# Kernel tuning notes

Hardware: AMD Instinct MI355X
Metric: run time of the kernel (lower is better)

The kernel has to match this reference:

```python
import jax, jax.numpy as jnp
import numpy as np

N = 20000          # total nodes across batched graphs
E_REL = 60000      # edges per relation type (3 relation types)
N_CLASSES = 32
NUM_GRAPHS = 64
HEADS = 8
OUT_CH = 48
FUSED = 384        # 3 * 128 fused node feature dim
EPS = 1e-5         # PyG LayerNorm eps
NEG_SLOPE = 0.2    # RGATConv leaky_relu slope
NUM_ITERS = 2


def setup_inputs() -> dict:
    key = jax.random.key(0)
    ks = iter(jax.random.split(key, 48))

    def nrm(shape, scale=0.05):
        return jax.random.normal(next(ks), shape, jnp.float32) * scale

    inp = {}
    inp["x_visual"] = jax.random.normal(next(ks), (N, 1024), jnp.float32)
    inp["x_geom"] = jax.random.normal(next(ks), (N, 6), jnp.float32)
    inp["x_prior"] = jax.random.uniform(next(ks), (N, N_CLASSES + 1), jnp.float32)
    inp["edge_index_overlap"] = jax.random.randint(next(ks), (2, E_REL), 0, N)
    inp["edge_index_arch"] = jax.random.randint(next(ks), (2, E_REL), 0, N)
    inp["edge_index_spatial"] = jax.random.randint(next(ks), (2, E_REL), 0, N)
    inp["batch"] = jnp.sort(jax.random.randint(next(ks), (N,), 0, NUM_GRAPHS))
    # encoders: Linear -> ReLU -> PyG LayerNorm(graph mode, batch=None)
    inp["vis_W"] = nrm((1024, 128)); inp["vis_b"] = jnp.zeros((128,), jnp.float32)
    inp["vis_lnw"] = jnp.ones((128,), jnp.float32); inp["vis_lnb"] = jnp.zeros((128,), jnp.float32)
    inp["geo_W"] = nrm((6, 128)); inp["geo_b"] = jnp.zeros((128,), jnp.float32)
    inp["geo_lnw"] = jnp.ones((128,), jnp.float32); inp["geo_lnb"] = jnp.zeros((128,), jnp.float32)
    inp["pri_W"] = nrm((N_CLASSES + 1, 128)); inp["pri_b"] = jnp.zeros((128,), jnp.float32)
    inp["pri_lnw"] = jnp.ones((128,), jnp.float32); inp["pri_lnb"] = jnp.zeros((128,), jnp.float32)
    # RGATConv params: weight (R, in, H*O), q/k (H*O, H*dim) with dim=1, bias (H*O)
    for i in (1, 2):
        inp[f"rgat{i}_W"] = nrm((3, FUSED, HEADS * OUT_CH))
        inp[f"rgat{i}_q"] = nrm((HEADS * OUT_CH, HEADS))
        inp[f"rgat{i}_k"] = nrm((HEADS * OUT_CH, HEADS))
        inp[f"rgat{i}_bias"] = jnp.zeros((HEADS * OUT_CH,), jnp.float32)
        inp[f"n{i}_w"] = jnp.ones((FUSED,), jnp.float32)
        inp[f"n{i}_b"] = jnp.zeros((FUSED,), jnp.float32)
    inp["cls_W1"] = nrm((FUSED, 128)); inp["cls_b1"] = jnp.zeros((128,), jnp.float32)
    inp["cls_W2"] = nrm((128, N_CLASSES)); inp["cls_b2"] = jnp.zeros((N_CLASSES,), jnp.float32)
    return inp


def _encoder(x, W, b, lnw, lnb):
    # Linear -> ReLU -> PyG LayerNorm(mode='graph', batch=None): scalar mean/std
    h = jax.nn.relu(x @ W + b)
    h = h - h.mean()
    h = h / (h.std() + EPS)
    return h * lnw + lnb


def _graph_layernorm(x, batch, w, b):
    # PyG LayerNorm(mode='graph') with batch vector: normalize per graph over nodes*channels
    cnt = jax.ops.segment_sum(jnp.ones((x.shape[0],), x.dtype), batch, NUM_GRAPHS)
    norm = jnp.clip(cnt, 1.0, None) * x.shape[-1]
    mean = jax.ops.segment_sum(x, batch, NUM_GRAPHS).sum(-1) / norm
    xc = x - mean[batch][:, None]
    var = jax.ops.segment_sum(xc * xc, batch, NUM_GRAPHS).sum(-1) / norm
    out = xc / jnp.sqrt(var + EPS)[batch][:, None]
    return out * w + b


def _rgat(x, src, dst, etype, W, q, k, bias):
    # RGATConv: additive self-attention, across-relation softmax, concat heads, sum aggr
    n = x.shape[0]
    xr = jnp.einsum('nf,rfo->rno', x, W)          # per-relation node transform (R,N,H*O)
    outi = xr[etype, dst]                          # (E, H*O) transformed dst features
    outj = xr[etype, src]                          # (E, H*O) transformed src features
    alpha = jax.nn.leaky_relu(outi @ q + outj @ k, NEG_SLOPE)  # (E, H)
    amax = jax.ops.segment_max(alpha, dst, n)
    amax = jnp.where(jnp.isfinite(amax), amax, 0.0)
    ex = jnp.exp(alpha - amax[dst])
    den = jax.ops.segment_sum(ex, dst, n)
    a = ex / (den[dst] + 1e-16)                    # per-dst-node softmax over all relations
    msg = (a[:, :, None] * outj.reshape(-1, HEADS, OUT_CH)).reshape(-1, HEADS * OUT_CH)
    return jax.ops.segment_sum(msg, dst, n) + bias


def reference(x_visual, x_geom, x_prior, edge_index_overlap, edge_index_arch,
              edge_index_spatial, batch, vis_W, vis_b, vis_lnw, vis_lnb,
              geo_W, geo_b, geo_lnw, geo_lnb, pri_W, pri_b, pri_lnw, pri_lnb,
              rgat1_W, rgat1_q, rgat1_k, rgat1_bias, n1_w, n1_b,
              rgat2_W, rgat2_q, rgat2_k, rgat2_bias, n2_w, n2_b,
              cls_W1, cls_b1, cls_W2, cls_b2):
    ei = jnp.concatenate([edge_index_overlap, edge_index_arch, edge_index_spatial], axis=1)
    src, dst = ei[0], ei[1]
    etype = jnp.concatenate([jnp.full((E_REL,), r, jnp.int32) for r in range(3)])

    h_vis = _encoder(x_visual, vis_W, vis_b, vis_lnw, vis_lnb)
    h_geo = _encoder(x_geom, geo_W, geo_b, geo_lnw, geo_lnb)

    cur_prior = x_prior
    logits = None
    for t in range(NUM_ITERS):
        h_pri = _encoder(cur_prior, pri_W, pri_b, pri_lnw, pri_lnb)
        h0 = jnp.concatenate([h_vis, h_geo, h_pri], axis=-1)  # (N, 384)
        h1 = jax.nn.elu(_rgat(h0, src, dst, etype, rgat1_W, rgat1_q, rgat1_k, rgat1_bias)) + h0
        h1 = _graph_layernorm(h1, batch, n1_w, n1_b)
        h2 = jax.nn.elu(_rgat(h1, src, dst, etype, rgat2_W, rgat2_q, rgat2_k, rgat2_bias)) + h1
        h2 = _graph_layernorm(h2, batch, n2_w, n2_b)
        logits = jax.nn.relu(h2 @ cls_W1 + cls_b1) @ cls_W2 + cls_b2  # dropout off (eval)
        if t < NUM_ITERS - 1:
            probs = jax.nn.softmax(logits, axis=-1)
            cur_prior = jnp.concatenate([probs, probs.max(-1, keepdims=True)], axis=-1)
    return logits
```

## Files before the change

### kernel.cpp

```cpp
#include <hip/hip_runtime.h>
#include <hip/hip_bf16.h>

#define Nn 20000
#define EREL 60000
#define ETOT 180000
#define NG 64
#define FD 384
#define EPS 1e-5f

typedef unsigned short u16;
typedef unsigned int u32;
typedef __attribute__((ext_vector_type(8))) short s8v;
typedef __attribute__((ext_vector_type(4))) float f4v;

static inline int cdiv(int a, int b) { return (a + b - 1) / b; }

__device__ inline u16 f2b(float f) {
    __hip_bfloat16 h = __float2bfloat16(f);
    union { __hip_bfloat16 b; u16 u; } c; c.b = h; return c.u;
}
__device__ inline float b2f(u16 u) {
    union { __hip_bfloat16 b; u16 u; } c; c.u = u; return __bfloat162float(c.b);
}

__global__ __launch_bounds__(256) void split_k(const float* __restrict__ x,
    u16* __restrict__ hi, u16* __restrict__ lo, int n4)
{
    int i = blockIdx.x * 256 + threadIdx.x;
    if (i >= n4) return;
    float4 v = ((const float4*)x)[i];
    ushort4 h, l;
    h.x = f2b(v.x); l.x = f2b(v.x - b2f(h.x));
    h.y = f2b(v.y); l.y = f2b(v.y - b2f(h.y));
    h.z = f2b(v.z); l.z = f2b(v.z - b2f(h.z));
    h.w = f2b(v.w); l.w = f2b(v.w - b2f(h.w));
    ((ushort4*)hi)[i] = h;
    ((ushort4*)lo)[i] = l;
}

__global__ void tsplit_k(const float* __restrict__ W, u16* __restrict__ hi,
                         u16* __restrict__ lo, int K, int N, int total)
{
    int idx = blockIdx.x * 256 + threadIdx.x;
    if (idx >= total) return;
    int kn = K * N;
    int b = idx / kn, rem = idx - b * kn;
    int k = rem / N, n = rem - k * N;
    float v = W[idx];
    u16 h = f2b(v), l = f2b(v - b2f(h));
    int o = b * kn + n * K + k;
    hi[o] = h; lo[o] = l;
}

__global__ void prep_qkw_k(const float* __restrict__ q, const float* __restrict__ kk,
                           u16* __restrict__ hi, u16* __restrict__ lo)
{
    int idx = blockIdx.x * 256 + threadIdx.x;
    if (idx >= 16 * 384) return;
    int col = idx / 384, k = idx - col * 384;
    float v = (col < 8) ? q[k * 8 + col] : kk[k * 8 + col - 8];
    u16 h = f2b(v), l = f2b(v - b2f(h));
    hi[idx] = h; lo[idx] = l;
}

#define USEI(i) ((i) < 2 || ((i) >= 4 && (i) < 6) || (TERMS >= 2 && ((i) == 2 || (i) == 3)) || (TERMS >= 3 && (i) >= 6))
template<bool BIAS, bool RELU, bool STATS, bool OB16, int TERMS, bool SWZ>
__global__ __launch_bounds__(256) void mgemm_k(
    const u16* __restrict__ Ahi, const u16* __restrict__ Alo,
    const u16* __restrict__ Bhi, const u16* __restrict__ Blo,
    const float* __restrict__ bias, void* __restrict__ Cv,
    int M, int K, int ldc, int bstride, float* __restrict__ stats)
{
    __shared__ u16 lds[4 * 128 * 32];
    __shared__ float red[256];
    const int t = threadIdx.x;
    int brow, bcol, z;
    if (SWZ) {
        int d = blockIdx.x;
        int xcd = d & 7, s = d >> 3;
        int row = xcd + 8 * (s / 9);
        int c = s % 9;
        brow = row * 128;
        if (brow >= M) return;
        bcol = (c % 3) * 128;
        z = c / 3;
    } else {
        brow = blockIdx.x * 128; bcol = blockIdx.y * 128; z = blockIdx.z;
    }
    Bhi += (size_t)z * bstride;
    Blo += (size_t)z * bstride;
    float* Cf = OB16 ? nullptr : (float*)Cv + (size_t)z * M * ldc;
    u16*   Ch = OB16 ? (u16*)Cv + (size_t)z * M * ldc : nullptr;

    const int r0 = t >> 2, sl = t & 3;
    const int rA0 = min(brow + r0, M - 1);
// ... 65 lines not shown
    float s1 = 0.f, s2 = 0.f;
    #pragma unroll
    for (int tm = 0; tm < 4; tm++) {
        #pragma unroll
        for (int rg = 0; rg < 4; rg++) {
            int row = brow + wr + tm * 16 + kq * 4 + rg;
            if (row < M) {
                #pragma unroll
                for (int tn = 0; tn < 4; tn++) {
                    int col = bcol + wc + tn * 16 + lr;
                    float v = acc[tm][tn][rg];
                    if (BIAS) v += bias[col];
                    if (RELU) v = fmaxf(v, 0.f);
                    if (OB16) Ch[(size_t)row * ldc + col] = f2b(v);
                    else      Cf[(size_t)row * ldc + col] = v;
                    if (STATS) { s1 += v; s2 += v * v; }
                }
            }
        }
    }
    if (STATS) {
        __syncthreads();
        red[t] = s1; __syncthreads();
        for (int o = 128; o; o >>= 1) { if (t < o) red[t] += red[t + o]; __syncthreads(); }
        if (t == 0) atomicAdd(&stats[0], red[0]);
        __syncthreads();
        red[t] = s2; __syncthreads();
        for (int o = 128; o; o >>= 1) { if (t < o) red[t] += red[t + o]; __syncthreads(); }
        if (t == 0) atomicAdd(&stats[1], red[0]);
    }
}
#undef USEI

__global__ __launch_bounds__(256) void proj_k(const u16* __restrict__ xr,
    const u16* __restrict__ qkw_hi, const u16* __restrict__ qkw_lo,
    float* __restrict__ qik)
{
    const int M3 = 3 * Nn;
    __shared__ u16 a_lds[128 * 32];
    __shared__ u16 b_lds[2][16 * 392];
    int t = threadIdx.x;
    int brow = blockIdx.x * 128;

    for (int i = t; i < 768; i += 256) {
        int col = i / 48, c8 = (i - col * 48) * 8;
        *(s8v*)&b_lds[0][col * 392 + c8] = *(const s8v*)(qkw_hi + col * 384 + c8);
        *(s8v*)&b_lds[1][col * 392 + c8] = *(const s8v*)(qkw_lo + col * 384 + c8);
    }

    int ar = t >> 1;
    int sl0 = (t & 1) * 2;
    int grow = min(brow + ar, M3 - 1);
    const u16* asrc = xr + (size_t)grow * 384;
    int adst0 = ar * 32 + ((sl0 ^ (ar & 3)) << 3);
    int adst1 = ar * 32 + (((sl0 + 1) ^ (ar & 3)) << 3);

    int l = t & 63, w = t >> 6;
    int lr = l & 15, kq = l >> 4;
    f4v acc0 = {}, acc1 = {};

    s8v stg0 = *(const s8v*)(asrc + sl0 * 8);
    s8v stg1 = *(const s8v*)(asrc + sl0 * 8 + 8);
    for (int kc = 0; kc < 12; kc++) {
        if (kc) __syncthreads();
        *(s8v*)&a_lds[adst0] = stg0;
        *(s8v*)&a_lds[adst1] = stg1;
        __syncthreads();
        if (kc + 1 < 12) {
            int ko = (kc + 1) * 32 + sl0 * 8;
            stg0 = *(const s8v*)(asrc + ko);
            stg1 = *(const s8v*)(asrc + ko + 8);
        }
        s8v bh = *(const s8v*)&b_lds[0][lr * 392 + kc * 32 + kq * 8];
        s8v bl = *(const s8v*)&b_lds[1][lr * 392 + kc * 32 + kq * 8];
        int r0 = w * 32 + lr;
        s8v a0 = *(const s8v*)&a_lds[r0 * 32 + ((kq ^ (r0 & 3)) << 3)];
        int r1 = r0 + 16;
        s8v a1 = *(const s8v*)&a_lds[r1 * 32 + ((kq ^ (r1 & 3)) << 3)];
        acc0 = __builtin_amdgcn_mfma_f32_16x16x32_bf16(a0, bh, acc0, 0, 0, 0);
        acc0 = __builtin_amdgcn_mfma_f32_16x16x32_bf16(a0, bl, acc0, 0, 0, 0);
        acc1 = __builtin_amdgcn_mfma_f32_16x16x32_bf16(a1, bh, acc1, 0, 0, 0);
        acc1 = __builtin_amdgcn_mfma_f32_16x16x32_bf16(a1, bl, acc1, 0, 0, 0);
    }
    #pragma unroll
    for (int rg = 0; rg < 4; rg++) {
        int row0 = brow + w * 32 + kq * 4 + rg;
        if (row0 < M3) qik[(size_t)row0 * 16 + lr] = acc0[rg];
        int row1 = row0 + 16;
        if (row1 < M3) qik[(size_t)row1 * 16 + lr] = acc1[rg];
    }
}

template<bool BIAS, bool RELU, bool STATS>
__global__ __launch_bounds__(256) void sgemm_k(
    const float* __restrict__ A, const float* __restrict__ B,
    const float* __restrict__ bias, float* __restrict__ C,
    int M, int K, int N, int ldc, float* __restrict__ stats)
{
    const int BK = 16;
    const int r = blockIdx.z;
    B += (size_t)r * K * N;
    C += (size_t)r * M * ldc;
    __shared__ float As[16][65];
    __shared__ float Bs[16][64];
    int tid = threadIdx.x;
    int tx = tid & 15, ty = tid >> 4;
    int brow = blockIdx.x * 64, bcol = blockIdx.y * 64;
    float acc[4][4] = {};
    for (int k0 = 0; k0 < K; k0 += BK) {
        #pragma unroll
        for (int i = 0; i < 4; i++) {
            int e = tid + 256 * i;
            int ar = e >> 4, ak = e & 15;
            int gr = brow + ar, gk = k0 + ak;
            As[ak][ar] = (gr < M && gk < K) ? A[(size_t)gr * K + gk] : 0.f;
            int bk = e >> 6, bn = e & 63;
            int gbk = k0 + bk, gbn = bcol + bn;
            Bs[bk][bn] = (gbk < K && gbn < N) ? B[(size_t)gbk * N + gbn] : 0.f;
        }
        __syncthreads();
        #pragma unroll
        for (int k = 0; k < BK; k++) {
            float ra[4], rb[4];
// ... 29 lines not shown
        __shared__ float red[256];
        __syncthreads();
        red[tid] = s1; __syncthreads();
        for (int o = 128; o; o >>= 1) { if (tid < o) red[tid] += red[tid + o]; __syncthreads(); }
        if (tid == 0) atomicAdd(&stats[0], red[0]);
        __syncthreads();
        red[tid] = s2; __syncthreads();
        for (int o = 128; o; o >>= 1) { if (tid < o) red[tid] += red[tid + o]; __syncthreads(); }
        if (tid == 0) atomicAdd(&stats[1], red[0]);
    }
}

__global__ __launch_bounds__(256) void enc_norm_k(const float* __restrict__ H,
                           const float* __restrict__ w, const float* __restrict__ b,
                           const float* __restrict__ stats, float cntinv, u16* __restrict__ hi)
{
    int i = blockIdx.x * 256 + threadIdx.x;
    if (i >= Nn * 32) return;
    int n = i >> 5, c4 = i & 31;
    float m = stats[0] * cntinv;
    float var = stats[1] * cntinv - m * m;
    float s = 1.f / (sqrtf(fmaxf(var, 0.f)) + EPS);
    float4 wv = ((const float4*)w)[c4];
    float4 bv = ((const float4*)b)[c4];
    float4 v = ((const float4*)(H + (size_t)n * FD))[c4];
    ushort4 hh;
    hh.x = f2b((v.x - m) * s * wv.x + bv.x);
    hh.y = f2b((v.y - m) * s * wv.y + bv.y);
    hh.z = f2b((v.z - m) * s * wv.z + bv.z);
    hh.w = f2b((v.w - m) * s * wv.w + bv.w);
    ((ushort4*)(hi + (size_t)n * FD))[c4] = hh;
}

__global__ __launch_bounds__(256) void ew_k(const float* __restrict__ qik,
    const int* __restrict__ eidx, const int* __restrict__ dste, float* __restrict__ ew)
{
    int e = blockIdx.x * 256 + threadIdx.x;
    if (e >= ETOT) return;
    int p = eidx[e];
    int src = p & 0xFFFFFF, et = p >> 24;
    int dst = dste[e];
    const float4* q4 = (const float4*)(qik + ((size_t)et * Nn + dst) * 16);
    const float4* k4 = (const float4*)(qik + ((size_t)et * Nn + src) * 16 + 8);
    float4 out[2];
    #pragma unroll
    for (int half = 0; half < 2; half++) {
        float4 qv = q4[half], kv = k4[half];
        float a0 = qv.x + kv.x, a1 = qv.y + kv.y, a2 = qv.z + kv.z, a3 = qv.w + kv.w;
        a0 = (a0 > 0.f) ? a0 : 0.2f * a0;
        a1 = (a1 > 0.f) ? a1 : 0.2f * a1;
        a2 = (a2 > 0.f) ? a2 : 0.2f * a2;
        a3 = (a3 > 0.f) ? a3 : 0.2f * a3;
        out[half] = make_float4(__expf(a0), __expf(a1), __expf(a2), __expf(a3));
    }
    float4* ew4 = (float4*)(ew + (size_t)e * 8);
    ew4[0] = out[0];
    ew4[1] = out[1];
}

__global__ void edge_count_k(const int* __restrict__ e0, const int* __restrict__ e1,
                             const int* __restrict__ e2, int* __restrict__ cnt)
{
    int e = blockIdx.x * 256 + threadIdx.x;
    if (e >= ETOT) return;
    int r = e / EREL, i = e - r * EREL;
    const int* ei = (r == 0) ? e0 : (r == 1) ? e1 : e2;
    atomicAdd(&cnt[ei[EREL + i]], 1);
}

__global__ void edge_fill_k(const int* __restrict__ e0, const int* __restrict__ e1,
                            const int* __restrict__ e2, int* __restrict__ cursor,
                            int* __restrict__ eidx, int* __restrict__ dste)
{
    int e = blockIdx.x * 256 + threadIdx.x;
    if (e >= ETOT) return;
    int r = e / EREL, i = e - r * EREL;
    const int* ei = (r == 0) ? e0 : (r == 1) ? e1 : e2;
    int src = ei[i], dst = ei[EREL + i];
    int pos = atomicAdd(&cursor[dst], 1);
    eidx[pos] = src | (r << 24);
    dste[pos] = dst;
}

__global__ __launch_bounds__(1024) void scan_k(const int* __restrict__ cnt,
                                               int* __restrict__ rowptr, int* __restrict__ cursor)
{
    __shared__ int wsum[16], wpre[16];
    __shared__ int carry, tot;
    int t = threadIdx.x, lane = t & 63, wid = t >> 6;
    if (t == 0) carry = 0;
    __syncthreads();
    for (int base = 0; base < Nn; base += 1024) {
        int i = base + t;
        int v = (i < Nn) ? cnt[i] : 0;
        int s = v;
        #pragma unroll
        for (int o = 1; o < 64; o <<= 1) {
            int x = __shfl_up(s, o);
            if (lane >= o) s += x;
        }
        if (lane == 63) wsum[wid] = s;
        __syncthreads();
        if (t < 16) {
            int wv = wsum[t];
            int ws = wv;
            #pragma unroll
            for (int o = 1; o < 16; o <<= 1) {
                int x = __shfl_up(ws, o);
                if (t >= o) ws += x;
            }
            wpre[t] = ws - wv;
            if (t == 15) tot = ws;
        }
        __syncthreads();
        if (i < Nn) {
            int ex = carry + wpre[wid] + s - v;
            rowptr[i] = ex; cursor[i] = ex;
        }
        __syncthreads();
        if (t == 0) carry += tot;
    }
    __syncthreads();
    if (t == 0) rowptr[Nn] = carry;
}

__global__ __launch_bounds__(256) void gcount_k(const int* __restrict__ batch, int* __restrict__ gcnt)
{
    __shared__ int bins[NG];
    int t = threadIdx.x;
    if (t < NG) bins[t] = 0;
    __syncthreads();
    int n = blockIdx.x * 256 + t;
    if (n < Nn) atomicAdd(&bins[batch[n]], 1);
    __syncthreads();
    if (t < NG && bins[t]) atomicAdd(&gcnt[t], bins[t]);
}

__global__ __launch_bounds__(256) void aggr_k(const u16* __restrict__ xr,
    const float* __restrict__ ew, const int* __restrict__ rowptr, const int* __restrict__ eidx,
    const float* __restrict__ bias, const u16* __restrict__ hinb,
    const int* __restrict__ batch, u16* __restrict__ outb,
    float* __restrict__ gsum, float* __restrict__ gsq)
{
    __shared__ float ls[NG], lq[NG];
    int t = threadIdx.x;
    if (t < NG) { ls[t] = 0.f; lq[t] = 0.f; }
    __syncthreads();
    int node = blockIdx.x * 4 + (t >> 6);
    int lane = t & 63;
    int e0 = rowptr[node], e1 = rowptr[node + 1];
    int hd[3];
    #pragma unroll
    for (int j = 0; j < 3; j++) hd[j] = (lane * 2 + 128 * j) / 48;
    float den = 0.f;
    float accx[3] = {}, accy[3] = {};

    int e = e0;
    while (e + 4 <= e1) {
        int p0 = eidx[e], p1 = eidx[e + 1], p2 = eidx[e + 2], p3 = eidx[e + 3];
        const u32* r0 = (const u32*)(xr + ((size_t)(p0 >> 24) * Nn + (p0 & 0xFFFFFF)) * FD);
        const u32* r1 = (const u32*)(xr + ((size_t)(p1 >> 24) * Nn + (p1 & 0xFFFFFF)) * FD);
        const u32* r2 = (const u32*)(xr + ((size_t)(p2 >> 24) * Nn + (p2 & 0xFFFFFF)) * FD);
        const u32* r3 = (const u32*)(xr + ((size_t)(p3 >> 24) * Nn + (p3 & 0xFFFFFF)) * FD);
        float ev0 = (lane < 8) ? ew[(size_t)e * 8 + lane] : 0.f;
        float ev1 = (lane < 8) ? ew[(size_t)(e + 1) * 8 + lane] : 0.f;
        float ev2 = (lane < 8) ? ew[(size_t)(e + 2) * 8 + lane] : 0.f;
        float ev3 = (lane < 8) ? ew[(size_t)(e + 3) * 8 + lane] : 0.f;
        u32 u0[3], u1[3], u2[3], u3[3];
        #pragma unroll
        for (int j = 0; j < 3; j++) u0[j] = r0[lane + 64 * j];
        #pragma unroll
        for (int j = 0; j < 3; j++) u1[j] = r1[lane + 64 * j];
        #pragma unroll
        for (int j = 0; j < 3; j++) u2[j] = r2[lane + 64 * j];
        #pragma unroll
        for (int j = 0; j < 3; j++) u3[j] = r3[lane + 64 * j];
        den += ev0 + ev1 + ev2 + ev3;
        #pragma unroll
        for (int j = 0; j < 3; j++) {
            float a0 = __shfl(ev0, hd[j]), a1 = __shfl(ev1, hd[j]);
            float a2 = __shfl(ev2, hd[j]), a3 = __shfl(ev3, hd[j]);
            accx[j] = fmaf(a0, __uint_as_float(u0[j] << 16), accx[j]);
            accy[j] = fmaf(a0, __uint_as_float(u0[j] & 0xffff0000u), accy[j]);
            accx[j] = fmaf(a1, __uint_as_float(u1[j] << 16), accx[j]);
            accy[j] = fmaf(a1, __uint_as_float(u1[j] & 0xffff0000u), accy[j]);
            accx[j] = fmaf(a2, __uint_as_float(u2[j] << 16), accx[j]);
            accy[j] = fmaf(a2, __uint_as_float(u2[j] & 0xffff0000u), accy[j]);
            accx[j] = fmaf(a3, __uint_as_float(u3[j] << 16), accx[j]);
            accy[j] = fmaf(a3, __uint_as_float(u3[j] & 0xffff0000u), accy[j]);
        }
        e += 4;
    }
    for (; e < e1; e++) {
        int p = eidx[e];
        int srcn = p & 0xFFFFFF, et = p >> 24;
        float ev = (lane < 8) ? ew[(size_t)e * 8 + lane] : 0.f;
        den += ev;
        const u32* row = (const u32*)(xr + ((size_t)et * Nn + srcn) * FD);
        #pragma unroll
        for (int j = 0; j < 3; j++) {
            float a = __shfl(ev, hd[j]);
            u32 u = row[lane + 64 * j];
            accx[j] = fmaf(a, __uint_as_float(u << 16), accx[j]);
            accy[j] = fmaf(a, __uint_as_float(u & 0xffff0000u), accy[j]);
        }
    }

    float s1 = 0.f, s2 = 0.f;
    #pragma unroll
    for (int j = 0; j < 3; j++) {
        float dh = __shfl(den, hd[j]);
        float rcp = 1.f / (dh + 1e-16f);
        int c = lane * 2 + 128 * j;
        float2 bv = *(const float2*)(bias + c);
        u32 hb = ((const u32*)(hinb + (size_t)node * FD))[lane + 64 * j];
        float vx = accx[j] * rcp + bv.x;
        float vy = accy[j] * rcp + bv.y;
        vx = (vx > 0.f) ? vx : expm1f(vx);
        vy = (vy > 0.f) ? vy : expm1f(vy);
        vx += b2f((u16)(hb & 0xffffu));
        vy += b2f((u16)(hb >> 16));
        u32 pb = (u32)f2b(vx) | ((u32)f2b(vy) << 16);
        ((u32*)(outb + (size_t)node * FD))[lane + 64 * j] = pb;
        s1 += vx + vy; s2 += vx * vx + vy * vy;
    }
    #pragma unroll
    for (int o = 32; o; o >>= 1) { s1 += __shfl_down(s1, o); s2 += __shfl_down(s2, o); }
    int g = batch[node];
    if (lane == 0) { atomicAdd(&ls[g], s1); atomicAdd(&lq[g], s2); }
    __syncthreads();
    if (t < NG && (ls[t] != 0.f || lq[t] != 0.f)) {
        atomicAdd(&gsum[t], ls[t]);
        atomicAdd(&gsq[t], lq[t]);
    }
}

template<bool WLO>
__global__ __launch_bounds__(256) void gnorm_split_k(const u16* __restrict__ yb,
    const int* __restrict__ batch, const float* __restrict__ gsum, const float* __restrict__ gsq,
    const int* __restrict__ gcnt, const float* __restrict__ w, const float* __restrict__ b,
    u16* __restrict__ hi, u16* __restrict__ lo)
{
    int i = blockIdx.x * 256 + threadIdx.x;
    if (i >= Nn * (FD / 4)) return;
    int n = i / 96;
    int c4 = i - n * 96;
    int g = batch[n];
    float norm = fmaxf((float)gcnt[g], 1.f) * (float)FD;
    float m = gsum[g] / norm;
    float var = gsq[g] / norm - m * m;
    float rstd = rsqrtf(var + EPS);
    float4 wv = ((const float4*)w)[c4];
    float4 bv = ((const float4*)b)[c4];
    uint2 yv = ((const uint2*)yb)[i];
    float v0 = (b2f((u16)(yv.x & 0xffffu)) - m) * rstd * wv.x + bv.x;
    float v1 = (b2f((u16)(yv.x >> 16))     - m) * rstd * wv.y + bv.y;
// ... 34 lines not shown
                              hipStream_t stream)
{
    const float* x_visual = (const float*)d_in[0];
    const float* x_geom   = (const float*)d_in[1];
    const float* x_prior  = (const float*)d_in[2];
    const int* ei0   = (const int*)d_in[3];
    const int* ei1   = (const int*)d_in[4];
    const int* ei2   = (const int*)d_in[5];
    const int* batch = (const int*)d_in[6];
    const float* vis_W = (const float*)d_in[7];  const float* vis_b = (const float*)d_in[8];
    const float* vis_lnw = (const float*)d_in[9]; const float* vis_lnb = (const float*)d_in[10];
    const float* geo_W = (const float*)d_in[11]; const float* geo_b = (const float*)d_in[12];
    const float* geo_lnw = (const float*)d_in[13]; const float* geo_lnb = (const float*)d_in[14];
    const float* pri_W = (const float*)d_in[15]; const float* pri_b = (const float*)d_in[16];
    const float* pri_lnw = (const float*)d_in[17]; const float* pri_lnb = (const float*)d_in[18];
    const float* rgat_W[2]    = { (const float*)d_in[19], (const float*)d_in[25] };
    const float* rgat_q[2]    = { (const float*)d_in[20], (const float*)d_in[26] };
    const float* rgat_kk[2]   = { (const float*)d_in[21], (const float*)d_in[27] };
    const float* rgat_bias[2] = { (const float*)d_in[22], (const float*)d_in[28] };
    const float* ln_w[2]      = { (const float*)d_in[23], (const float*)d_in[29] };
    const float* ln_b[2]      = { (const float*)d_in[24], (const float*)d_in[30] };
    const float* cls_W1 = (const float*)d_in[31]; const float* cls_b1 = (const float*)d_in[32];
    const float* cls_W2 = (const float*)d_in[33]; const float* cls_b2 = (const float*)d_in[34];
    float* OUT = (float*)d_out;

    float* ws = (float*)d_ws;
    float* XRreg = ws;
    u16*   XR16  = (u16*)XRreg;
    float* HCAT  = XRreg + (size_t)3 * Nn * FD;
    float* HA    = HCAT + (size_t)Nn * FD;
    float* HB    = HA + (size_t)Nn * FD;
    float* PRIOR = HB + (size_t)Nn * FD;
    float* QIK   = PRIOR + (size_t)Nn * 33;
    u16* HS0_HI  = (u16*)(QIK + (size_t)3 * Nn * 16);
    u16* HS0_LO  = HS0_HI + (size_t)Nn * FD;
    u16* HS1_HI  = HS0_LO + (size_t)Nn * FD;
    u16* HS1_LO  = HS1_HI + (size_t)Nn * FD;
    u16* RW_HI   = HS1_LO + (size_t)Nn * FD;
    u16* RW_LO   = RW_HI + (size_t)2 * 3 * 384 * 384;
    u16* VW_HI   = RW_LO + (size_t)2 * 3 * 384 * 384;
    u16* VW_LO   = VW_HI + (size_t)128 * 1024;
    u16* CW_HI   = VW_LO + (size_t)128 * 1024;
    u16* CW_LO   = CW_HI + (size_t)128 * 384;
    u16* QKW_HI  = CW_LO + (size_t)128 * 384;
    u16* QKW_LO  = QKW_HI + (size_t)2 * 16 * 384;
    float* STATS = (float*)(QKW_LO + (size_t)2 * 16 * 384);
    float* GSUM  = STATS + 2;
    float* GSQ   = GSUM + 64;
    int* CNT    = (int*)(GSQ + 64);
    int* ROWPTR = CNT + Nn;
    int* CURSOR = ROWPTR + Nn + 1;
    int* EIDX   = CURSOR + Nn;
    int* GCNT   = EIDX + ETOT;
    int* DSTE   = GCNT + 64;
    float* EW   = (float*)(DSTE + ETOT);
    u16* VA_HI = (u16*)XRreg;
    u16* VA_LO = VA_HI + (size_t)Nn * 1024;
    float* CLSH = XRreg;
    u16* HS2_HI = (u16*)(XRreg + (size_t)12 * 1000 * 1000);
    u16* HS2_LO = HS2_HI + (size_t)Nn * FD;
    u16* YB0 = (u16*)HA;
    u16* YB1 = (u16*)HB;

    hipMemsetAsync(CNT, 0, Nn * sizeof(int), stream);
    edge_count_k<<<cdiv(ETOT, 256), 256, 0, stream>>>(ei0, ei1, ei2, CNT);
    scan_k<<<1, 1024, 0, stream>>>(CNT, ROWPTR, CURSOR);
    edge_fill_k<<<cdiv(ETOT, 256), 256, 0, stream>>>(ei0, ei1, ei2, CURSOR, EIDX, DSTE);
    hipMemsetAsync(GCNT, 0, 64 * sizeof(int), stream);
    gcount_k<<<cdiv(Nn, 256), 256, 0, stream>>>(batch, GCNT);

    tsplit_k<<<cdiv(3 * 384 * 384, 256), 256, 0, stream>>>(rgat_W[0], RW_HI, RW_LO, 384, 384, 3 * 384 * 384);
    tsplit_k<<<cdiv(3 * 384 * 384, 256), 256, 0, stream>>>(rgat_W[1], RW_HI + 3 * 384 * 384, RW_LO + 3 * 384 * 384, 384, 384, 3 * 384 * 384);
    tsplit_k<<<cdiv(1024 * 128, 256), 256, 0, stream>>>(vis_W, VW_HI, VW_LO, 1024, 128, 1024 * 128);
    tsplit_k<<<cdiv(384 * 128, 256), 256, 0, stream>>>(cls_W1, CW_HI, CW_LO, 384, 128, 384 * 128);
    prep_qkw_k<<<cdiv(16 * 384, 256), 256, 0, stream>>>(rgat_q[0], rgat_kk[0], QKW_HI, QKW_LO);
    prep_qkw_k<<<cdiv(16 * 384, 256), 256, 0, stream>>>(rgat_q[1], rgat_kk[1], QKW_HI + 16 * 384, QKW_LO + 16 * 384);
    split_k<<<cdiv(Nn * 1024 / 4, 256), 256, 0, stream>>>(x_visual, VA_HI, VA_LO, Nn * 1024 / 4);

    const int MB = cdiv(Nn, 128);
    const int XRBLK = 160 * 9;

    hipMemsetAsync(STATS, 0, 2 * sizeof(float), stream);
    mgemm_k<true, true, true, false, 2, false><<<dim3(MB, 1, 1), 256, 0, stream>>>(
        VA_HI, VA_LO, VW_HI, VW_LO, vis_b, HCAT, Nn, 1024, FD, 0, STATS);
    enc_norm_k<<<cdiv(Nn * 32, 256), 256, 0, stream>>>(HCAT, vis_lnw, vis_lnb, STATS, 1.f / ((float)Nn * 128.f), HS0_HI);

    dim3 genc(cdiv(Nn, 64), 2, 1);
    hipMemsetAsync(STATS, 0, 2 * sizeof(float), stream);
    sgemm_k<true, true, true><<<genc, 256, 0, stream>>>(x_geom, geo_W, geo_b, HCAT + 128, Nn, 6, 128, FD, STATS);
    enc_norm_k<<<cdiv(Nn * 32, 256), 256, 0, stream>>>(HCAT + 128, geo_lnw, geo_lnb, STATS, 1.f / ((float)Nn * 128.f), HS0_HI + 128);

    for (int t = 0; t < 2; t++) {
        const float* pin = t ? PRIOR : x_prior;
        hipMemsetAsync(STATS, 0, 2 * sizeof(float), stream);
        sgemm_k<true, true, true><<<genc, 256, 0, stream>>>(pin, pri_W, pri_b, HCAT + 256, Nn, 33, 128, FD, STATS);
        enc_norm_k<<<cdiv(Nn * 32, 256), 256, 0, stream>>>(HCAT + 256, pri_lnw, pri_lnb, STATS, 1.f / ((float)Nn * 128.f), HS0_HI + 256);

        for (int L = 0; L < 2; L++) {
            const u16* ahi = L ? HS1_HI : HS0_HI;
            const u16* alo = L ? HS1_LO : HS0_LO;
            u16* yout = L ? YB1 : YB0;
            mgemm_k<false, false, false, true, 1, true><<<dim3(XRBLK, 1, 1), 256, 0, stream>>>(
                ahi, alo, RW_HI + (size_t)L * 3 * 384 * 384, RW_LO + (size_t)L * 3 * 384 * 384,
                nullptr, XR16, Nn, 384, FD, 384 * 384, nullptr);
            proj_k<<<cdiv(3 * Nn, 128), 256, 0, stream>>>(XR16,
                QKW_HI + (size_t)L * 16 * 384, QKW_LO + (size_t)L * 16 * 384, QIK);
            ew_k<<<cdiv(ETOT, 256), 256, 0, stream>>>(QIK, EIDX, DSTE, EW);
            hipMemsetAsync(GSUM, 0, 128 * sizeof(float), stream);
            aggr_k<<<cdiv(Nn, 4), 256, 0, stream>>>(XR16, EW, ROWPTR, EIDX, rgat_bias[L],
                                                    ahi, batch, yout, GSUM, GSQ);
            if (L == 0)
                gnorm_split_k<false><<<cdiv(Nn * 96, 256), 256, 0, stream>>>(
                    YB0, batch, GSUM, GSQ, GCNT, ln_w[0], ln_b[0], HS1_HI, HS1_LO);
            else
                gnorm_split_k<true><<<cdiv(Nn * 96, 256), 256, 0, stream>>>(
                    YB1, batch, GSUM, GSQ, GCNT, ln_w[1], ln_b[1], HS2_HI, HS2_LO);
        }

        mgemm_k<true, true, false, false, 3, false><<<dim3(MB, 1, 1), 256, 0, stream>>>(
            HS2_HI, HS2_LO, CW_HI, CW_LO, cls_b1, CLSH, Nn, 384, 128, 0, nullptr);
        sgemm_k<true, false, false><<<dim3(cdiv(Nn, 64), 1, 1), 256, 0, stream>>>(
            CLSH, cls_W2, cls_b2, OUT, Nn, 128, 32, 32, nullptr);

        if (t == 0)
            softmax_prior_k<<<cdiv(Nn, 8), 256, 0, stream>>>(OUT, PRIOR);
    }
}
```

Before: 803.8 us.

## Fold q/k into RGAT weights, fuse edge scores into aggregation, drop lo-splits

Precomputes W·q and W·k per relation so the attention projections come straight from the input features (projh_k) rather than from the transformed features. The separate per-edge weight kernel and its dst array are removed, and attention logits and exponentials are now computed inside the aggregation kernel. The aggregation also switches to a contiguous lane*3 feature layout. Low bf16 residual splits are dropped for the visual input and RGAT weights, and the visual GEMM goes from two terms to one, which cuts preprocessing and GEMM work at some cost in precision.

```diff
diff --git a/kernel.cpp b/kernel.cpp
--- a/kernel.cpp
+++ b/kernel.cpp
@@ -23,21 +23,27 @@
     union { __hip_bfloat16 b; u16 u; } c; c.u = u; return __bfloat162float(c.b);
 }
 
+template<bool WLO>
 __global__ __launch_bounds__(256) void split_k(const float* __restrict__ x,
     u16* __restrict__ hi, u16* __restrict__ lo, int n4)
 {
     int i = blockIdx.x * 256 + threadIdx.x;
     if (i >= n4) return;
     float4 v = ((const float4*)x)[i];
-    ushort4 h, l;
-    h.x = f2b(v.x); l.x = f2b(v.x - b2f(h.x));
-    h.y = f2b(v.y); l.y = f2b(v.y - b2f(h.y));
-    h.z = f2b(v.z); l.z = f2b(v.z - b2f(h.z));
-    h.w = f2b(v.w); l.w = f2b(v.w - b2f(h.w));
+    ushort4 h;
+    h.x = f2b(v.x); h.y = f2b(v.y); h.z = f2b(v.z); h.w = f2b(v.w);
     ((ushort4*)hi)[i] = h;
-    ((ushort4*)lo)[i] = l;
-}
-
+    if (WLO) {
+        ushort4 l;
+        l.x = f2b(v.x - b2f(h.x));
+        l.y = f2b(v.y - b2f(h.y));
+        l.z = f2b(v.z - b2f(h.z));
+        l.w = f2b(v.w - b2f(h.w));
+        ((ushort4*)lo)[i] = l;
+    }
+}
+
+template<bool WLO>
 __global__ void tsplit_k(const float* __restrict__ W, u16* __restrict__ hi,
                          u16* __restrict__ lo, int K, int N, int total)
 {
@@ -47,20 +53,33 @@
     int b = idx / kn, rem = idx - b * kn;
     int k = rem / N, n = rem - k * N;
     float v = W[idx];
-    u16 h = f2b(v), l = f2b(v - b2f(h));
+    u16 h = f2b(v);
     int o = b * kn + n * K + k;
-    hi[o] = h; lo[o] = l;
-}
-
-__global__ void prep_qkw_k(const float* __restrict__ q, const float* __restrict__ kk,
-                           u16* __restrict__ hi, u16* __restrict__ lo)
+    hi[o] = h;
+    if (WLO) lo[o] = f2b(v - b2f(h));
+}
+
+__global__ __launch_bounds__(256) void w2_k(const float* __restrict__ W0,
+    const float* __restrict__ q0, const float* __restrict__ k0,
+    const float* __restrict__ W1, const float* __restrict__ q1, const float* __restrict__ k1,
+    u16* __restrict__ hi, u16* __restrict__ lo)
 {
     int idx = blockIdx.x * 256 + threadIdx.x;
-    if (idx >= 16 * 384) return;
-    int col = idx / 384, k = idx - col * 384;
-    float v = (col < 8) ? q[k * 8 + col] : kk[k * 8 + col - 8];
-    u16 h = f2b(v), l = f2b(v - b2f(h));
-    hi[idx] = h; lo[idx] = l;
+    if (idx >= 2 * 3 * 384 * 16) return;
+    int c = idx & 15;
+    int rest = idx >> 4;
+    int kin = rest % 384;
+    int lr3 = rest / 384;
+    int L = lr3 / 3, r = lr3 - L * 3;
+    const float* W = (L ? W1 : W0) + ((size_t)r * 384 + kin) * 384;
+    const float* qm = (c < 8) ? (L ? q1 : q0) : (L ? k1 : k0);
+    int h = c & 7;
+    float s = 0.f;
+    for (int d = 0; d < 384; d++) s = fmaf(W[d], qm[d * 8 + h], s);
+    u16 hh = f2b(s);
+    size_t o = ((size_t)L * 48 + r * 16 + c) * 384 + kin;
+    hi[o] = hh;
+    lo[o] = f2b(s - b2f(hh));
 }
 
 #define USEI(i) ((i) < 2 || ((i) >= 4 && (i) < 6) || (TERMS >= 2 && ((i) == 2 || (i) == 3)) || (TERMS >= 3 && (i) >= 6))
@@ -192,32 +211,29 @@
 }
 #undef USEI
 
-__global__ __launch_bounds__(256) void proj_k(const u16* __restrict__ xr,
-    const u16* __restrict__ qkw_hi, const u16* __restrict__ qkw_lo,
-    float* __restrict__ qik)
-{
-    const int M3 = 3 * Nn;
+__global__ __launch_bounds__(256) void projh_k(const u16* __restrict__ hs,
+    const u16* __restrict__ w2hi, const u16* __restrict__ w2lo, float* __restrict__ qik)
+{
     __shared__ u16 a_lds[128 * 32];
-    __shared__ u16 b_lds[2][16 * 392];
+    __shared__ u16 b_lds[2][48 * 392];
     int t = threadIdx.x;
     int brow = blockIdx.x * 128;
 
-    for (int i = t; i < 768; i += 256) {
+    for (int i = t; i < 2304; i += 256) {
         int col = i / 48, c8 = (i - col * 48) * 8;
-        *(s8v*)&b_lds[0][col * 392 + c8] = *(const s8v*)(qkw_hi + col * 384 + c8);
-        *(s8v*)&b_lds[1][col * 392 + c8] = *(const s8v*)(qkw_lo + col * 384 + c8);
-    }
-
-    int ar = t >> 1;
-    int sl0 = (t & 1) * 2;
-    int grow = min(brow + ar, M3 - 1);
-    const u16* asrc = xr + (size_t)grow * 384;
+        *(s8v*)&b_lds[0][col * 392 + c8] = *(const s8v*)(w2hi + col * 384 + c8);
+        *(s8v*)&b_lds[1][col * 392 + c8] = *(const s8v*)(w2lo + col * 384 + c8);
+    }
+
+    int ar = t >> 1, sl0 = (t & 1) * 2;
+    int grow = min(brow + ar, Nn - 1);
+    const u16* asrc = hs + (size_t)grow * FD;
     int adst0 = ar * 32 + ((sl0 ^ (ar & 3)) << 3);
     int adst1 = ar * 32 + (((sl0 + 1) ^ (ar & 3)) << 3);
 
     int l = t & 63, w = t >> 6;
     int lr = l & 15, kq = l >> 4;
-    f4v acc0 = {}, acc1 = {};
+    f4v acc[2][3] = {};
 
     s8v stg0 = *(const s8v*)(asrc + sl0 * 8);
     s8v stg1 = *(const s8v*)(asrc + sl0 * 8 + 8);
@@ -231,24 +247,32 @@
             stg0 = *(const s8v*)(asrc + ko);
             stg1 = *(const s8v*)(asrc + ko + 8);
         }
-        s8v bh = *(const s8v*)&b_lds[0][lr * 392 + kc * 32 + kq * 8];
-        s8v bl = *(const s8v*)&b_lds[1][lr * 392 + kc * 32 + kq * 8];
-        int r0 = w * 32 + lr;
-        s8v a0 = *(const s8v*)&a_lds[r0 * 32 + ((kq ^ (r0 & 3)) << 3)];
-        int r1 = r0 + 16;
-        s8v a1 = *(const s8v*)&a_lds[r1 * 32 + ((kq ^ (r1 & 3)) << 3)];
-        acc0 = __builtin_amdgcn_mfma_f32_16x16x32_bf16(a0, bh, acc0, 0, 0, 0);
-        acc0 = __builtin_amdgcn_mfma_f32_16x16x32_bf16(a0, bl, acc0, 0, 0, 0);
-        acc1 = __builtin_amdgcn_mfma_f32_16x16x32_bf16(a1, bh, acc1, 0, 0, 0);
-        acc1 = __builtin_amdgcn_mfma_f32_16x16x32_bf16(a1, bl, acc1, 0, 0, 0);
-    }
-    #pragma unroll
-    for (int rg = 0; rg < 4; rg++) {
-        int row0 = brow + w * 32 + kq * 4 + rg;
-        if (row0 < M3) qik[(size_t)row0 * 16 + lr] = acc0[rg];
-        int row1 = row0 + 16;
-        if (row1 < M3) qik[(size_t)row1 * 16 + lr] = acc1[rg];
-    }
+        s8v bh[3], bl[3];
+        #pragma unroll
+        for (int cf = 0; cf < 3; cf++) {
+            bh[cf] = *(const s8v*)&b_lds[0][(cf * 16 + lr) * 392 + kc * 32 + kq * 8];
+            bl[cf] = *(const s8v*)&b_lds[1][(cf * 16 + lr) * 392 + kc * 32 + kq * 8];
+        }
+        #pragma unroll
+        for (int rf = 0; rf < 2; rf++) {
+            int rr = w * 32 + rf * 16 + lr;
+            s8v a = *(const s8v*)&a_lds[rr * 32 + ((kq ^ (rr & 3)) << 3)];
+            #pragma unroll
+            for (int cf = 0; cf < 3; cf++) {
+                acc[rf][cf] = __builtin_amdgcn_mfma_f32_16x16x32_bf16(a, bh[cf], acc[rf][cf], 0, 0, 0);
+                acc[rf][cf] = __builtin_amdgcn_mfma_f32_16x16x32_bf16(a, bl[cf], acc[rf][cf], 0, 0, 0);
+            }
+        }
+    }
+    #pragma unroll
+    for (int rf = 0; rf < 2; rf++)
+        #pragma unroll
+        for (int cf = 0; cf < 3; cf++)
+            #pragma unroll
+            for (int rg = 0; rg < 4; rg++) {
+                int row = brow + w * 32 + rf * 16 + kq * 4 + rg;
+                if (row < Nn) qik[(size_t)row * 48 + cf * 16 + lr] = acc[rf][cf][rg];
+            }
 }
 
 template<bool BIAS, bool RELU, bool STATS>
@@ -344,32 +368,6 @@
     ((ushort4*)(hi + (size_t)n * FD))[c4] = hh;
 }
 
-__global__ __launch_bounds__(256) void ew_k(const float* __restrict__ qik,
-    const int* __restrict__ eidx, const int* __restrict__ dste, float* __restrict__ ew)
-{
-    int e = blockIdx.x * 256 + threadIdx.x;
-    if (e >= ETOT) return;
-    int p = eidx[e];
-    int src = p & 0xFFFFFF, et = p >> 24;
-    int dst = dste[e];
-    const float4* q4 = (const float4*)(qik + ((size_t)et * Nn + dst) * 16);
-    const float4* k4 = (const float4*)(qik + ((size_t)et * Nn + src) * 16 + 8);
-    float4 out[2];
-    #pragma unroll
-    for (int half = 0; half < 2; half++) {
-        float4 qv = q4[half], kv = k4[half];
-        float a0 = qv.x + kv.x, a1 = qv.y + kv.y, a2 = qv.z + kv.z, a3 = qv.w + kv.w;
-        a0 = (a0 > 0.f) ? a0 : 0.2f * a0;
-        a1 = (a1 > 0.f) ? a1 : 0.2f * a1;
-        a2 = (a2 > 0.f) ? a2 : 0.2f * a2;
-        a3 = (a3 > 0.f) ? a3 : 0.2f * a3;
-        out[half] = make_float4(__expf(a0), __expf(a1), __expf(a2), __expf(a3));
-    }
-    float4* ew4 = (float4*)(ew + (size_t)e * 8);
-    ew4[0] = out[0];
-    ew4[1] = out[1];
-}
-
 __global__ void edge_count_k(const int* __restrict__ e0, const int* __restrict__ e1,
                              const int* __restrict__ e2, int* __restrict__ cnt)
 {
@@ -382,7 +380,7 @@
 
 __global__ void edge_fill_k(const int* __restrict__ e0, const int* __restrict__ e1,
                             const int* __restrict__ e2, int* __restrict__ cursor,
-                            int* __restrict__ eidx, int* __restrict__ dste)
+                            int* __restrict__ eidx)
 {
     int e = blockIdx.x * 256 + threadIdx.x;
     if (e >= ETOT) return;
@@ -391,7 +389,6 @@
     int src = ei[i], dst = ei[EREL + i];
     int pos = atomicAdd(&cursor[dst], 1);
     eidx[pos] = src | (r << 24);
-    dste[pos] = dst;
 }
 
 __global__ __launch_bounds__(1024) void scan_k(const int* __restrict__ cnt,
@@ -449,7 +446,7 @@
 }
 
 __global__ __launch_bounds__(256) void aggr_k(const u16* __restrict__ xr,
-    const float* __restrict__ ew, const int* __restrict__ rowptr, const int* __restrict__ eidx,
+    const float* __restrict__ qik, const int* __restrict__ rowptr, const int* __restrict__ eidx,
     const float* __restrict__ bias, const u16* __restrict__ hinb,
     const int* __restrict__ batch, u16* __restrict__ outb,
     float* __restrict__ gsum, float* __restrict__ gsq)
@@ -461,79 +458,99 @@
     int node = blockIdx.x * 4 + (t >> 6);
     int lane = t & 63;
     int e0 = rowptr[node], e1 = rowptr[node + 1];
-    int hd[3];
-    #pragma unroll
-    for (int j = 0; j < 3; j++) hd[j] = (lane * 2 + 128 * j) / 48;
+    int hd = lane >> 3;
+    float qv = (lane < 48) ? qik[(size_t)node * 48 + lane] : 0.f;
     float den = 0.f;
-    float accx[3] = {}, accy[3] = {};
+    float acc[6] = {};
 
     int e = e0;
     while (e + 4 <= e1) {
         int p0 = eidx[e], p1 = eidx[e + 1], p2 = eidx[e + 2], p3 = eidx[e + 3];
-        const u32* r0 = (const u32*)(xr + ((size_t)(p0 >> 24) * Nn + (p0 & 0xFFFFFF)) * FD);
-        const u32* r1 = (const u32*)(xr + ((size_t)(p1 >> 24) * Nn + (p1 & 0xFFFFFF)) * FD);
-        const u32* r2 = (const u32*)(xr + ((size_t)(p2 >> 24) * Nn + (p2 & 0xFFFFFF)) * FD);
-        const u32* r3 = (const u32*)(xr + ((size_t)(p3 >> 24) * Nn + (p3 & 0xFFFFFF)) * FD);
-        float ev0 = (lane < 8) ? ew[(size_t)e * 8 + lane] : 0.f;
-        float ev1 = (lane < 8) ? ew[(size_t)(e + 1) * 8 + lane] : 0.f;
-        float ev2 = (lane < 8) ? ew[(size_t)(e + 2) * 8 + lane] : 0.f;
-        float ev3 = (lane < 8) ? ew[(size_t)(e + 3) * 8 + lane] : 0.f;
+        int n0 = p0 & 0xFFFFFF, et0 = p0 >> 24;
+        int n1 = p1 & 0xFFFFFF, et1 = p1 >> 24;
+        int n2 = p2 & 0xFFFFFF, et2 = p2 >> 24;
+        int n3 = p3 & 0xFFFFFF, et3 = p3 >> 24;
+        float kv0 = (lane < 8) ? qik[(size_t)n0 * 48 + et0 * 16 + 8 + lane] : 0.f;
+        float kv1 = (lane < 8) ? qik[(size_t)n1 * 48 + et1 * 16 + 8 + lane] : 0.f;
+        float kv2 = (lane < 8) ? qik[(size_t)n2 * 48 + et2 * 16 + 8 + lane] : 0.f;
+        float kv3 = (lane < 8) ? qik[(size_t)n3 * 48 + et3 * 16 + 8 + lane] : 0.f;
+        const u32* r0 = (const u32*)(xr + ((size_t)et0 * Nn + n0) * FD);
+        const u32* r1 = (const u32*)(xr + ((size_t)et1 * Nn + n1) * FD);
+        const u32* r2 = (const u32*)(xr + ((size_t)et2 * Nn + n2) * FD);
+        const u32* r3 = (const u32*)(xr + ((size_t)et3 * Nn + n3) * FD);
         u32 u0[3], u1[3], u2[3], u3[3];
         #pragma unroll
-        for (int j = 0; j < 3; j++) u0[j] = r0[lane + 64 * j];
-        #pragma unroll
-        for (int j = 0; j < 3; j++) u1[j] = r1[lane + 64 * j];
-        #pragma unroll
-        for (int j = 0; j < 3; j++) u2[j] = r2[lane + 64 * j];
-        #pragma unroll
-        for (int j = 0; j < 3; j++) u3[j] = r3[lane + 64 * j];
-        den += ev0 + ev1 + ev2 + ev3;
+        for (int j = 0; j < 3; j++) u0[j] = r0[lane * 3 + j];
+        #pragma unroll
+        for (int j = 0; j < 3; j++) u1[j] = r1[lane * 3 + j];
+        #pragma unroll
+        for (int j = 0; j < 3; j++) u2[j] = r2[lane * 3 + j];
+        #pragma unroll
+        for (int j = 0; j < 3; j++) u3[j] = r3[lane * 3 + j];
+        float qq0 = __shfl(qv, et0 * 16 + (lane & 7));
+        float qq1 = __shfl(qv, et1 * 16 + (lane & 7));
+        float qq2 = __shfl(qv, et2 * 16 + (lane & 7));
+        float qq3 = __shfl(qv, et3 * 16 + (lane & 7));
+        float ex0 = 0.f, ex1 = 0.f, ex2 = 0.f, ex3 = 0.f;
+        if (lane < 8) {
+            float a0 = qq0 + kv0; a0 = (a0 > 0.f) ? a0 : 0.2f * a0; ex0 = __expf(a0);
+            float a1 = qq1 + kv1; a1 = (a1 > 0.f) ? a1 : 0.2f * a1; ex1 = __expf(a1);
+            float a2 = qq2 + kv2; a2 = (a2 > 0.f) ? a2 : 0.2f * a2; ex2 = __expf(a2);
+            float a3 = qq3 + kv3; a3 = (a3 > 0.f) ? a3 : 0.2f * a3; ex3 = __expf(a3);
+        }
+        den += ex0 + ex1 + ex2 + ex3;
+        float w0 = __shfl(ex0, hd), w1 = __shfl(ex1, hd);
+        float w2 = __shfl(ex2, hd), w3 = __shfl(ex3, hd);
         #pragma unroll
         for (int j = 0; j < 3; j++) {
-            float a0 = __shfl(ev0, hd[j]), a1 = __shfl(ev1, hd[j]);
-            float a2 = __shfl(ev2, hd[j]), a3 = __shfl(ev3, hd[j]);
-            accx[j] = fmaf(a0, __uint_as_float(u0[j] << 16), accx[j]);
-            accy[j] = fmaf(a0, __uint_as_float(u0[j] & 0xffff0000u), accy[j]);
-            accx[j] = fmaf(a1, __uint_as_float(u1[j] << 16), accx[j]);
-            accy[j] = fmaf(a1, __uint_as_float(u1[j] & 0xffff0000u), accy[j]);
-            accx[j] = fmaf(a2, __uint_as_float(u2[j] << 16), accx[j]);
-            accy[j] = fmaf(a2, __uint_as_float(u2[j] & 0xffff0000u), accy[j]);
-            accx[j] = fmaf(a3, __uint_as_float(u3[j] << 16), accx[j]);
-            accy[j] = fmaf(a3, __uint_as_float(u3[j] & 0xffff0000u), accy[j]);
+            acc[2*j]   = fmaf(w0, __uint_as_float(u0[j] << 16), acc[2*j]);
+            acc[2*j+1] = fmaf(w0, __uint_as_float(u0[j] & 0xffff0000u), acc[2*j+1]);
+            acc[2*j]   = fmaf(w1, __uint_as_float(u1[j] << 16), acc[2*j]);
+            acc[2*j+1] = fmaf(w1, __uint_as_float(u1[j] & 0xffff0000u), acc[2*j+1]);
+            acc[2*j]   = fmaf(w2, __uint_as_float(u2[j] << 16), acc[2*j]);
+            acc[2*j+1] = fmaf(w2, __uint_as_float(u2[j] & 0xffff0000u), acc[2*j+1]);
+            acc[2*j]   = fmaf(w3, __uint_as_float(u3[j] << 16), acc[2*j]);
+            acc[2*j+1] = fmaf(w3, __uint_as_float(u3[j] & 0xffff0000u), acc[2*j+1]);
         }
         e += 4;
     }
     for (; e < e1; e++) {
         int p = eidx[e];
-        int srcn = p & 0xFFFFFF, et = p >> 24;
-        float ev = (lane < 8) ? ew[(size_t)e * 8 + lane] : 0.f;
-        den += ev;
-        const u32* row = (const u32*)(xr + ((size_t)et * Nn + srcn) * FD);
+        int sn = p & 0xFFFFFF, et = p >> 24;
+        float kv = (lane < 8) ? qik[(size_t)sn * 48 + et * 16 + 8 + lane] : 0.f;
+        const u32* rr = (const u32*)(xr + ((size_t)et * Nn + sn) * FD);
+        u32 u[3];
+        #pragma unroll
+        for (int j = 0; j < 3; j++) u[j] = rr[lane * 3 + j];
+        float qq = __shfl(qv, et * 16 + (lane & 7));
+        float ex = 0.f;
+        if (lane < 8) { float a = qq + kv; a = (a > 0.f) ? a : 0.2f * a; ex = __expf(a); }
+        den += ex;
+        float wv_ = __shfl(ex, hd);
         #pragma unroll
         for (int j = 0; j < 3; j++) {
-            float a = __shfl(ev, hd[j]);
-            u32 u = row[lane + 64 * j];
-            accx[j] = fmaf(a, __uint_as_float(u << 16), accx[j]);
-            accy[j] = fmaf(a, __uint_as_float(u & 0xffff0000u), accy[j]);
-        }
-    }
-
+            acc[2*j]   = fmaf(wv_, __uint_as_float(u[j] << 16), acc[2*j]);
+            acc[2*j+1] = fmaf(wv_, __uint_as_float(u[j] & 0xffff0000u), acc[2*j+1]);
+        }
+    }
+
+    float dh = __shfl(den, hd);
+    float rcp = 1.f / (dh + 1e-16f);
+    const u32* hp = (const u32*)(hinb + (size_t)node * FD);
+    u32* op = (u32*)(outb + (size_t)node * FD);
     float s1 = 0.f, s2 = 0.f;
     #pragma unroll
     for (int j = 0; j < 3; j++) {
-        float dh = __shfl(den, hd[j]);
-        float rcp = 1.f / (dh + 1e-16f);
-        int c = lane * 2 + 128 * j;
+        int c = lane * 6 + 2 * j;
         float2 bv = *(const float2*)(bias + c);
-        u32 hb = ((const u32*)(hinb + (size_t)node * FD))[lane + 64 * j];
-        float vx = accx[j] * rcp + bv.x;
-        float vy = accy[j] * rcp + bv.y;
+        u32 hb = hp[lane * 3 + j];
+        float vx = acc[2*j] * rcp + bv.x;
+        float vy = acc[2*j+1] * rcp + bv.y;
         vx = (vx > 0.f) ? vx : expm1f(vx);
         vy = (vy > 0.f) ? vy : expm1f(vy);
         vx += b2f((u16)(hb & 0xffffu));
         vy += b2f((u16)(hb >> 16));
-        u32 pb = (u32)f2b(vx) | ((u32)f2b(vy) << 16);
-        ((u32*)(outb + (size_t)node * FD))[lane + 64 * j] = pb;
+        op[lane * 3 + j] = (u32)f2b(vx) | ((u32)f2b(vy) << 16);
         s1 += vx + vy; s2 += vx * vx + vy * vy;
     }
     #pragma unroll
@@ -634,7 +651,7 @@
     float* HB    = HA + (size_t)Nn * FD;
     float* PRIOR = HB + (size_t)Nn * FD;
     float* QIK   = PRIOR + (size_t)Nn * 33;
-    u16* HS0_HI  = (u16*)(QIK + (size_t)3 * Nn * 16);
+    u16* HS0_HI  = (u16*)(QIK + (size_t)Nn * 48);
     u16* HS0_LO  = HS0_HI + (size_t)Nn * FD;
     u16* HS1_HI  = HS0_LO + (size_t)Nn * FD;
     u16* HS1_LO  = HS1_HI + (size_t)Nn * FD;
@@ -644,9 +661,9 @@
     u16* VW_LO   = VW_HI + (size_t)128 * 1024;
     u16* CW_HI   = VW_LO + (size_t)128 * 1024;
     u16* CW_LO   = CW_HI + (size_t)128 * 384;
-    u16* QKW_HI  = CW_LO + (size_t)128 * 384;
-    u16* QKW_LO  = QKW_HI + (size_t)2 * 16 * 384;
-    float* STATS = (float*)(QKW_LO + (size_t)2 * 16 * 384);
+    u16* W2_HI   = CW_LO + (size_t)128 * 384;
+    u16* W2_LO   = W2_HI + (size_t)2 * 48 * 384;
+    float* STATS = (float*)(W2_LO + (size_t)2 * 48 * 384);
     float* GSUM  = STATS + 2;
     float* GSQ   = GSUM + 64;
     int* CNT    = (int*)(GSQ + 64);
@@ -654,10 +671,7 @@
     int* CURSOR = ROWPTR + Nn + 1;
     int* EIDX   = CURSOR + Nn;
     int* GCNT   = EIDX + ETOT;
-    int* DSTE   = GCNT + 64;
-    float* EW   = (float*)(DSTE + ETOT);
     u16* VA_HI = (u16*)XRreg;
-    u16* VA_LO = VA_HI + (size_t)Nn * 1024;
     float* CLSH = XRreg;
     u16* HS2_HI = (u16*)(XRreg + (size_t)12 * 1000 * 1000);
     u16* HS2_LO = HS2_HI + (size_t)Nn * FD;
@@ -667,24 +681,24 @@
     hipMemsetAsync(CNT, 0, Nn * sizeof(int), stream);
     edge_count_k<<<cdiv(ETOT, 256), 256, 0, stream>>>(ei0, ei1, ei2, CNT);
     scan_k<<<1, 1024, 0, stream>>>(CNT, ROWPTR, CURSOR);
-    edge_fill_k<<<cdiv(ETOT, 256), 256, 0, stream>>>(ei0, ei1, ei2, CURSOR, EIDX, DSTE);
+    edge_fill_k<<<cdiv(ETOT, 256), 256, 0, stream>>>(ei0, ei1, ei2, CURSOR, EIDX);
     hipMemsetAsync(GCNT, 0, 64 * sizeof(int), stream);
     gcount_k<<<cdiv(Nn, 256), 256, 0, stream>>>(batch, GCNT);
 
-    tsplit_k<<<cdiv(3 * 384 * 384, 256), 256, 0, stream>>>(rgat_W[0], RW_HI, RW_LO, 384, 384, 3 * 384 * 384);
-    tsplit_k<<<cdiv(3 * 384 * 384, 256), 256, 0, stream>>>(rgat_W[1], RW_HI + 3 * 384 * 384, RW_LO + 3 * 384 * 384, 384, 384, 3 * 384 * 384);
-    tsplit_k<<<cdiv(1024 * 128, 256), 256, 0, stream>>>(vis_W, VW_HI, VW_LO, 1024, 128, 1024 * 128);
-    tsplit_k<<<cdiv(384 * 128, 256), 256, 0, stream>>>(cls_W1, CW_HI, CW_LO, 384, 128, 384 * 128);
-    prep_qkw_k<<<cdiv(16 * 384, 256), 256, 0, stream>>>(rgat_q[0], rgat_kk[0], QKW_HI, QKW_LO);
-    prep_qkw_k<<<cdiv(16 * 384, 256), 256, 0, stream>>>(rgat_q[1], rgat_kk[1], QKW_HI + 16 * 384, QKW_LO + 16 * 384);
-    split_k<<<cdiv(Nn * 1024 / 4, 256), 256, 0, stream>>>(x_visual, VA_HI, VA_LO, Nn * 1024 / 4);
+    tsplit_k<false><<<cdiv(3 * 384 * 384, 256), 256, 0, stream>>>(rgat_W[0], RW_HI, RW_LO, 384, 384, 3 * 384 * 384);
+    tsplit_k<false><<<cdiv(3 * 384 * 384, 256), 256, 0, stream>>>(rgat_W[1], RW_HI + 3 * 384 * 384, RW_LO, 384, 384, 3 * 384 * 384);
+    tsplit_k<false><<<cdiv(1024 * 128, 256), 256, 0, stream>>>(vis_W, VW_HI, VW_LO, 1024, 128, 1024 * 128);
+    tsplit_k<true><<<cdiv(384 * 128, 256), 256, 0, stream>>>(cls_W1, CW_HI, CW_LO, 384, 128, 384 * 128);
+    w2_k<<<cdiv(2 * 3 * 384 * 16, 256), 256, 0, stream>>>(rgat_W[0], rgat_q[0], rgat_kk[0],
+        rgat_W[1], rgat_q[1], rgat_kk[1], W2_HI, W2_LO);
+    split_k<false><<<cdiv(Nn * 1024 / 4, 256), 256, 0, stream>>>(x_visual, VA_HI, nullptr, Nn * 1024 / 4);
 
     const int MB = cdiv(Nn, 128);
     const int XRBLK = 160 * 9;
 
     hipMemsetAsync(STATS, 0, 2 * sizeof(float), stream);
-    mgemm_k<true, true, true, false, 2, false><<<dim3(MB, 1, 1), 256, 0, stream>>>(
-        VA_HI, VA_LO, VW_HI, VW_LO, vis_b, HCAT, Nn, 1024, FD, 0, STATS);
+    mgemm_k<true, true, true, false, 1, false><<<dim3(MB, 1, 1), 256, 0, stream>>>(
+        VA_HI, VA_HI, VW_HI, VW_LO, vis_b, HCAT, Nn, 1024, FD, 0, STATS);
     enc_norm_k<<<cdiv(Nn * 32, 256), 256, 0, stream>>>(HCAT, vis_lnw, vis_lnb, STATS, 1.f / ((float)Nn * 128.f), HS0_HI);
 
     dim3 genc(cdiv(Nn, 64), 2, 1);
@@ -700,16 +714,14 @@
 
         for (int L = 0; L < 2; L++) {
             const u16* ahi = L ? HS1_HI : HS0_HI;
-            const u16* alo = L ? HS1_LO : HS0_LO;
             u16* yout = L ? YB1 : YB0;
             mgemm_k<false, false, false, true, 1, true><<<dim3(XRBLK, 1, 1), 256, 0, stream>>>(
-                ahi, alo, RW_HI + (size_t)L * 3 * 384 * 384, RW_LO + (size_t)L * 3 * 384 * 384,
+                ahi, ahi, RW_HI + (size_t)L * 3 * 384 * 384, RW_LO,
                 nullptr, XR16, Nn, 384, FD, 384 * 384, nullptr);
-            proj_k<<<cdiv(3 * Nn, 128), 256, 0, stream>>>(XR16,
-                QKW_HI + (size_t)L * 16 * 384, QKW_LO + (size_t)L * 16 * 384, QIK);
-            ew_k<<<cdiv(ETOT, 256), 256, 0, stream>>>(QIK, EIDX, DSTE, EW);
+            projh_k<<<MB, 256, 0, stream>>>(ahi,
+                W2_HI + (size_t)L * 48 * 384, W2_LO + (size_t)L * 48 * 384, QIK);
             hipMemsetAsync(GSUM, 0, 128 * sizeof(float), stream);
-            aggr_k<<<cdiv(Nn, 4), 256, 0, stream>>>(XR16, EW, ROWPTR, EIDX, rgat_bias[L],
+            aggr_k<<<cdiv(Nn, 4), 256, 0, stream>>>(XR16, QIK, ROWPTR, EIDX, rgat_bias[L],
                                                     ahi, batch, yout, GSUM, GSQ);
             if (L == 0)
                 gnorm_split_k<false><<<cdiv(Nn * 96, 256), 256, 0, stream>>>(
```

New measurement: 770.2 us. -4.2%, faster.
